# Kernel tuning notes

Hardware: AMD Instinct MI355X
Metric: run time of the kernel (lower is better)

Reference implementation:

```python
import jax, jax.numpy as jnp
import numpy as np

B, T, VG, S = 64, 256, 1232, 32
LW, VW = 64, 8000
N_TAGS = 8
BLANK = 0
IGNORE_INDEX = 0
TAG_FACTOR = 0.1
GLOSS_W = 1.0
WORD_W = 1.0
NEG = -1e30


def setup_inputs() -> dict:
    key = jax.random.key(0)
    k1, k2, k3, k4, k5, k6 = jax.random.split(key, 6)
    glosses = jax.random.randint(k1, (B, S), 1, VG)            # CTC targets (avoid blank=0)
    words = jax.random.randint(k2, (B, LW), 0, VW)             # translation targets
    glosses_scores = jax.random.normal(k3, (B, T, VG), jnp.float32)
    words_output = jax.nn.log_softmax(jax.random.normal(k4, (B, LW, VW), jnp.float32), axis=-1)
    frames_len = jnp.full((B,), T, jnp.int32)
    glosses_len = jax.random.randint(k5, (B,), 1, S + 1).astype(jnp.int32)
    tag_ids = jax.random.randint(k6, (VG,), 0, N_TAGS).astype(jnp.int32)
    return {"glosses": glosses, "words": words, "glosses_scores": glosses_scores,
            "words_output": words_output, "frames_len": frames_len,
            "glosses_len": glosses_len, "tag_ids": tag_ids}


def booster_scores(scores, tag_ids):
    # per-tag mean over vocab dim, gathered back per vocab entry
    onehot = jax.nn.one_hot(tag_ids, N_TAGS, dtype=scores.dtype)   # [V, n_tags]
    counts = onehot.sum(axis=0)                                    # [n_tags]
    tag_mean = jnp.einsum('btv,vn->btn', scores, onehot) / counts  # [B,T,n_tags]
    return scores + TAG_FACTOR * tag_mean[..., tag_ids]            # [B,T,V]


def ctc_loss_sum(log_probs, targets, input_lens, target_lens):
    # log_probs [B,T,V], targets [B,S]
    Bb, Tt, _ = log_probs.shape
    Ss = targets.shape[1]
    L = 2 * Ss + 1
    ext = jnp.full((Bb, L), BLANK, dtype=targets.dtype).at[:, 1::2].set(targets)  # blank-interleaved
    lp_ext = jnp.take_along_axis(log_probs, jnp.broadcast_to(ext[:, None, :], (Bb, Tt, L)), axis=2)  # [B,T,L]
    prev2 = jnp.pad(ext, ((0, 0), (2, 0)), constant_values=BLANK)[:, :L]
    can_skip = (ext != BLANK) & (ext != prev2)                    # [B,L]

    alpha0 = jnp.full((Bb, L), NEG, log_probs.dtype)
    alpha0 = alpha0.at[:, 0].set(lp_ext[:, 0, 0]).at[:, 1].set(lp_ext[:, 0, 1])

    lp_t = jnp.swapaxes(lp_ext, 0, 1)  # [T,B,L]

    def step(alpha, xs):
        lp, t = xs
        a1 = jnp.concatenate([jnp.full((Bb, 1), NEG, alpha.dtype), alpha[:, :-1]], axis=1)
        a2 = jnp.concatenate([jnp.full((Bb, 2), NEG, alpha.dtype), alpha[:, :-2]], axis=1)
        a2 = jnp.where(can_skip, a2, NEG)
        m = jnp.maximum(alpha, jnp.maximum(a1, a2))
        new = m + jnp.log(jnp.exp(alpha - m) + jnp.exp(a1 - m) + jnp.exp(a2 - m)) + lp
        valid = (t < input_lens)[:, None]
        return jnp.where(valid, new, alpha), None

    alpha, _ = jax.lax.scan(step, alpha0, (lp_t[1:], jnp.arange(1, Tt)))

    idx1 = 2 * target_lens.astype(jnp.int32)
    idx0 = jnp.maximum(idx1 - 1, 0)
    aN = jnp.take_along_axis(alpha, jnp.stack([idx0, idx1], axis=1), axis=1)  # [B,2]
    loss = -jax.nn.logsumexp(aN, axis=1)
    loss = jnp.where(loss > 1e29, 0.0, loss)  # zero_infinity
    return loss.sum()


def nll_loss_sum(log_probs, targets):
    # input = words_output.permute(0,2,1)[:,:,:-1], target = words[:,1:]
    lp = log_probs[:, :-1, :]          # [B, LW-1, VW]
    tgt = targets[:, 1:]               # [B, LW-1]
    g = jnp.take_along_axis(lp, tgt[..., None], axis=2)[..., 0]
    mask = tgt != IGNORE_INDEX
    return -jnp.where(mask, g, 0.0).sum()


def reference(glosses, words, glosses_scores, words_output, frames_len, glosses_len, tag_ids):
    boosted = booster_scores(glosses_scores, tag_ids)          # training=True path
    glosses_probs = jax.nn.log_softmax(boosted, axis=-1)
    recognition_loss = ctc_loss_sum(glosses_probs, glosses, frames_len, glosses_len)
    translation_loss = nll_loss_sum(words_output, words)
    total = GLOSS_W * recognition_loss + WORD_W * translation_loss
    return (total, recognition_loss, translation_loss)
```

## Files before the change

kernel.cpp:

```cpp
#include <hip/hip_runtime.h>

#define B_    64
#define T_    256
#define VG_   1232
#define S_    32
#define LW_   64
#define VW_   8000
#define NTAGS 8
#define NEG_  (-1e30f)
#define LP_STRIDE 34
#define LOG2E 1.44269504088896340736f
#define LN2   0.69314718055994530942f

__device__ __forceinline__ float exp2g(float x) {
    float r; asm("v_exp_f32 %0, %1" : "=v"(r) : "v"(x)); return r;
}
__device__ __forceinline__ float log2g(float x) {
    float r; asm("v_log_f32 %0, %1" : "=v"(r) : "v"(x)); return r;
}
__device__ __forceinline__ void st_agent(float* p, float v) {
    __hip_atomic_store(p, v, __ATOMIC_RELAXED, __HIP_MEMORY_SCOPE_AGENT);
}
__device__ __forceinline__ float ld_agent(const float* p) {
    return __hip_atomic_load(p, __ATOMIC_RELAXED, __HIP_MEMORY_SCOPE_AGENT);
}
__device__ __forceinline__ float dpp_shr1(float x, float fill) {
    int r = __builtin_amdgcn_update_dpp(
        __builtin_bit_cast(int, fill), __builtin_bit_cast(int, x),
        0x138, 0xF, 0xF, false);
    return __builtin_bit_cast(float, r);
}
template <int CTRL>
__device__ __forceinline__ float dpp_add(float x) {
    int s = __builtin_amdgcn_update_dpp(
        0, __builtin_bit_cast(int, x), CTRL, 0xF, 0xF, true);
    return x + __builtin_bit_cast(float, s);
}
__device__ __forceinline__ float wave_sum_to0(float x) {
    x = dpp_add<0x101>(x);
    x = dpp_add<0x102>(x);
    x = dpp_add<0x104>(x);
    x = dpp_add<0x108>(x);
    x += __shfl_xor(x, 16, 64);
    x += __shfl_xor(x, 32, 64);
    return x;
}

__global__ void k0_counts(const int* __restrict__ tag_ids,
                          float* __restrict__ invcnt2, int* __restrict__ counter) {
    __shared__ int c[NTAGS];
    if (threadIdx.x == 0) *counter = 0;
    if (threadIdx.x < NTAGS) c[threadIdx.x] = 0;
    __syncthreads();
    for (int v = threadIdx.x; v < VG_; v += 256)
        atomicAdd(&c[tag_ids[v]], 1);
    __syncthreads();
    if (threadIdx.x < NTAGS)
        invcnt2[threadIdx.x] = (0.1f * LOG2E) / (float)c[threadIdx.x];
}

__global__ __launch_bounds__(256) void kA_booster(
    const float* __restrict__ scores, const int* __restrict__ tag_ids,
    const int* __restrict__ glosses, const float* __restrict__ invcnt2,
    float* __restrict__ lp_ws)
{
    __shared__ float tm2L[4][NTAGS];
    const int tid  = threadIdx.x;
    const int lane = tid & 63;
    const int wv   = tid >> 6;
    const int row  = blockIdx.x * 4 + wv;
    const int b    = row >> 8;
    const float* srow = scores + (size_t)row * VG_;

    const int gidx = (lane >= 1 && lane < 33) ? glosses[b * S_ + lane - 1] : 0;

    float4 sv[5];
    int4   tv[5];
#pragma unroll
    for (int i = 0; i < 5; ++i) {
        const int idx = i * 64 + lane;
        const bool act = (i < 4) || (lane < 52);
        sv[i] = act ? ((const float4*)srow)[idx]  : make_float4(0.f, 0.f, 0.f, 0.f);
        tv[i] = act ? ((const int4*)tag_ids)[idx] : make_int4(0, 0, 0, 0);
    }
    const float gval = srow[gidx];
    const int   gtag = tag_ids[gidx];

    float sums[NTAGS];
#pragma unroll
    for (int n = 0; n < NTAGS; ++n) sums[n] = 0.f;
#pragma unroll
    for (int i = 0; i < 5; ++i) {
        const float xs[4] = {sv[i].x, sv[i].y, sv[i].z, sv[i].w};
        const int   ts[4] = {tv[i].x, tv[i].y, tv[i].z, tv[i].w};
#pragma unroll
        for (int j = 0; j < 4; ++j) {
#pragma unroll
            for (int n = 0; n < NTAGS; ++n)
                sums[n] += (ts[j] == n) ? xs[j] : 0.f;
        }
    }
#pragma unroll
    for (int n = 0; n < NTAGS; ++n) sums[n] = wave_sum_to0(sums[n]);

    if (lane == 0) {
#pragma unroll
        for (int n = 0; n < NTAGS; ++n)
            tm2L[wv][n] = sums[n] * invcnt2[n];
    }
    __builtin_amdgcn_sched_barrier(0);

    float se = 0.f;
#pragma unroll
    for (int i = 0; i < 5; ++i) {
        const float xs[4] = {sv[i].x, sv[i].y, sv[i].z, sv[i].w};
        const int   ts[4] = {tv[i].x, tv[i].y, tv[i].z, tv[i].w};
        const bool act = (i < 4) || (lane < 52);
#pragma unroll
        for (int j = 0; j < 4; ++j) {
            const float e = exp2g(fmaf(xs[j], LOG2E, tm2L[wv][ts[j]]));
            se += act ? e : 0.f;
        }
    }
    se = wave_sum_to0(se);
    const float se0 = __builtin_bit_cast(
        float, __builtin_amdgcn_readfirstlane(__builtin_bit_cast(int, se)));
    const float lse2 = log2g(se0);

    if (lane < 33) {
        const float v = fmaf(gval, LOG2E, tm2L[wv][gtag]) - lse2;
        lp_ws[(size_t)row * LP_STRIDE + lane] = v;
    }
}

template <bool FULL>
__device__ __forceinline__ void scan_body(
    const float* __restrict__ tile, int lane, int off, bool ok2, int Tlen,
    float& alpha, float& a64)
{
    auto STEP = [&](int t, float lp, float lpB) {
        const float a1 = dpp_shr1(alpha, NEG_);
        float a2 = dpp_shr1(a1, NEG_);
        a2 = ok2 ? a2 : NEG_;
        const float m3 = fmaxf(alpha, fmaxf(a1, a2));
        const float e0 = exp2g(alpha - m3);
        const float e1 = exp2g(a1 - m3);
        const float e2 = exp2g(a2 - m3);
        const float nw = (m3 + lp) + log2g((e0 + e1) + e2);
        const float m2 = fmaxf(a64, alpha);
        const float n64 = (m2 + lpB) + log2g(exp2g(a64 - m2) + exp2g(alpha - m2));
        if (FULL || t < Tlen) { alpha = nw; a64 = n64; }
    };

    float cur[4], curB[4];
#pragma unroll
    for (int j = 0; j < 4; ++j) {
        cur[j]  = tile[(1 + j) * LP_STRIDE + off];
        curB[j] = tile[(1 + j) * LP_STRIDE];
    }
    int tbase = 1;
    for (int g = 0; g < 63; ++g) {
        float nxt[4], nxtB[4];
        const int tb2 = tbase + 4;
#pragma unroll
        for (int j = 0; j < 4; ++j) {
            nxt[j]  = tile[(tb2 + j) * LP_STRIDE + off];
            nxtB[j] = tile[(tb2 + j) * LP_STRIDE];
        }
#pragma unroll
        for (int j = 0; j < 4; ++j) STEP(tbase + j, cur[j], curB[j]);
#pragma unroll
        for (int j = 0; j < 4; ++j) { cur[j] = nxt[j]; curB[j] = nxtB[j]; }
        tbase += 4;
    }
#pragma unroll
    for (int j = 0; j < 3; ++j) STEP(253 + j, cur[j], curB[j]);
}

__global__ __launch_bounds__(256) void kB_ctc_nll_final(
    const float* __restrict__ lp_ws, const int* __restrict__ glosses,
    const int* __restrict__ frames_len, const int* __restrict__ glosses_len,
    const int* __restrict__ words, const float* __restrict__ words_out,
    float* __restrict__ loss_ws, float* __restrict__ nll_ws,
    int* __restrict__ counter, float* __restrict__ out)
{
    __shared__ __align__(16) float tile[(T_ + 1) * LP_STRIDE];
    const int tid = threadIdx.x;
    const int b   = blockIdx.x;

    float nacc = 0.f;
    if (tid < LW_ - 1) {
        const int tgt = words[b * LW_ + tid + 1];
        if (tgt != 0)
            nacc = -words_out[((size_t)b * LW_ + tid) * VW_ + tgt];
    }

    {
        const float4* src4 = (const float4*)(lp_ws + (size_t)b * T_ * LP_STRIDE);
        float4* dst4 = (float4*)tile;
        float4 r[9];
#pragma unroll
        for (int i = 0; i < 9; ++i) {
            const int idx = i * 256 + tid;
            if (idx < 2176) r[i] = src4[idx];
        }
#pragma unroll
        for (int i = 0; i < 9; ++i) {
            const int idx = i * 256 + tid;
            if (idx < 2176) dst4[idx] = r[i];
        }
    }
    __syncthreads();
    if (tid >= 64) return;
    const int lane = tid;

    const bool odd  = (lane & 1) != 0;
    const int  sIdx = (lane - 1) >> 1;
    bool ok2 = false;
    if (odd && sIdx >= 1) {
        const int g  = glosses[b * S_ + sIdx];
        const int gp = glosses[b * S_ + sIdx - 1];
        ok2 = (g != gp) && (g != 0);
    }
    const int off = odd ? (1 + sIdx) : 0;

    float alpha = NEG_;
    float a64   = NEG_;
    {
        const float lp00 = tile[off];
        if (lane <= 1) alpha = lp00;
    }
    const int Tlen = frames_len[b];

    if (Tlen == T_) scan_body<true >(tile, lane, off, ok2, Tlen, alpha, a64);
    else            scan_body<false>(tile, lane, off, ok2, Tlen, alpha, a64);

    const float a64v = __shfl(a64, 63, 64);
    const int i1 = 2 * glosses_len[b];
    const int i0 = i1 - 1;
    const float A0 = __shfl(alpha, i0, 64);
    const float A1 = (i1 >= 64) ? a64v : __shfl(alpha, i1, 64);
    const float mm = fmaxf(A0, A1);
    float loss = -(mm + log2g(exp2g(A0 - mm) + exp2g(A1 - mm))) * LN2;
    if (loss > 1e29f) loss = 0.f;

    nacc = wave_sum_to0(nacc);
    if (lane == 0) {
        st_agent(&loss_ws[b], loss);
        st_agent(&nll_ws[b], nacc);
    }

    asm volatile("s_waitcnt vmcnt(0)" ::: "memory");
    int old = 0;
    if (lane == 0) old = atomicAdd(counter, 1);
    old = __shfl(old, 0, 64);
    if (old == B_ - 1) {
        float v = ld_agent(&loss_ws[lane]);
        float u = ld_agent(&nll_ws[lane]);
#pragma unroll
        for (int o = 32; o >= 1; o >>= 1) {
            v += __shfl_xor(v, o, 64);
            u += __shfl_xor(u, o, 64);
        }
        if (lane == 0) {
            out[0] = v + u;
            out[1] = v;
            out[2] = u;
        }
    }
}

extern "C" void kernel_launch(void* const* d_in, const int* in_sizes, int n_in,
                              void* d_out, int out_size, void* d_ws, size_t ws_size,
                              hipStream_t stream) {
    const int*   glosses     = (const int*)d_in[0];
    const int*   words       = (const int*)d_in[1];
    const float* scores      = (const float*)d_in[2];
    const float* words_out   = (const float*)d_in[3];
    const int*   frames_len  = (const int*)d_in[4];
    const int*   glosses_len = (const int*)d_in[5];
    const int*   tag_ids     = (const int*)d_in[6];
    float* out = (float*)d_out;

    float* w       = (float*)d_ws;
    int*   counter = (int*)d_ws;
    float* invcnt2 = w + 8;
    float* loss_ws = w + 16;
    float* nll_ws  = w + 96;
    float* lp_ws   = w + 192;

    k0_counts<<<1, 256, 0, stream>>>(tag_ids, invcnt2, counter);
    kA_booster<<<(B_ * T_) / 4, 256, 0, stream>>>(scores, tag_ids, glosses,
                                                  invcnt2, lp_ws);
    kB_ctc_nll_final<<<B_, 256, 0, stream>>>(lp_ws, glosses, frames_len,
                                             glosses_len, words, words_out,
                                             loss_ws, nll_ws, counter, out);
}
```

Measured before the change: 52.19 us.

## Replace log-space CTC recursion with mantissa/exponent scaled probability-space scan

Rewrites the CTC alpha recursion to keep each state as a float mantissa plus an integer exponent in linear probability space, instead of log-space values. Each step now uses ldexp, add, multiply and frexp in place of several exp2 and log2 transcendental calls, which shortens the serial dependency chain of the latency-bound single-wave scan. Emission probabilities are exponentiated once as they are loaded. It adds integer DPP shifts and extra register state, and it changes numerical behaviour, so a NaN guard was added to the final loss.

```diff
diff --git a/kernel.cpp b/kernel.cpp
--- a/kernel.cpp
+++ b/kernel.cpp
@@ -8,6 +8,7 @@
 #define VW_   8000
 #define NTAGS 8
 #define NEG_  (-1e30f)
+#define RNEG  (-(1 << 28))
 #define LP_STRIDE 34
 #define LOG2E 1.44269504088896340736f
 #define LN2   0.69314718055994530942f
@@ -17,6 +18,15 @@
 }
 __device__ __forceinline__ float log2g(float x) {
     float r; asm("v_log_f32 %0, %1" : "=v"(r) : "v"(x)); return r;
+}
+__device__ __forceinline__ float ldexpg(float x, int e) {
+    float r; asm("v_ldexp_f32 %0, %1, %2" : "=v"(r) : "v"(x), "v"(e)); return r;
+}
+__device__ __forceinline__ float frexp_mantg(float x) {
+    float r; asm("v_frexp_mant_f32 %0, %1" : "=v"(r) : "v"(x)); return r;
+}
+__device__ __forceinline__ int frexp_expg(float x) {
+    int r; asm("v_frexp_exp_i32_f32 %0, %1" : "=v"(r) : "v"(x)); return r;
 }
 __device__ __forceinline__ void st_agent(float* p, float v) {
     __hip_atomic_store(p, v, __ATOMIC_RELAXED, __HIP_MEMORY_SCOPE_AGENT);
@@ -29,6 +39,9 @@
         __builtin_bit_cast(int, fill), __builtin_bit_cast(int, x),
         0x138, 0xF, 0xF, false);
     return __builtin_bit_cast(float, r);
+}
+__device__ __forceinline__ int dpp_shr1_i(int x, int fill) {
+    return __builtin_amdgcn_update_dpp(fill, x, 0x138, 0xF, 0xF, false);
 }
 template <int CTRL>
 __device__ __forceinline__ float dpp_add(float x) {
@@ -134,29 +147,34 @@
 }
 
 template <bool FULL>
-__device__ __forceinline__ void scan_body(
+__device__ __forceinline__ void scan_body_pls(
     const float* __restrict__ tile, int lane, int off, bool ok2, int Tlen,
-    float& alpha, float& a64)
+    float& mant, int& Rl, float& m64, int& R64)
 {
-    auto STEP = [&](int t, float lp, float lpB) {
-        const float a1 = dpp_shr1(alpha, NEG_);
-        float a2 = dpp_shr1(a1, NEG_);
-        a2 = ok2 ? a2 : NEG_;
-        const float m3 = fmaxf(alpha, fmaxf(a1, a2));
-        const float e0 = exp2g(alpha - m3);
-        const float e1 = exp2g(a1 - m3);
-        const float e2 = exp2g(a2 - m3);
-        const float nw = (m3 + lp) + log2g((e0 + e1) + e2);
-        const float m2 = fmaxf(a64, alpha);
-        const float n64 = (m2 + lpB) + log2g(exp2g(a64 - m2) + exp2g(alpha - m2));
-        if (FULL || t < Tlen) { alpha = nw; a64 = n64; }
+    auto STEP = [&](int t, float p, float pB) {
+        const float m1 = dpp_shr1(mant, 0.f);
+        const int   r1 = dpp_shr1_i(Rl, RNEG);
+        float m2 = dpp_shr1(m1, 0.f);
+        int   r2 = dpp_shr1_i(r1, RNEG);
+        m2 = ok2 ? m2 : 0.f;
+        r2 = ok2 ? r2 : RNEG;
+        const int rmax = max(Rl, max(r1, r2));
+        const float s  = ((ldexpg(mant, Rl - rmax) + ldexpg(m1, r1 - rmax))
+                          + ldexpg(m2, r2 - rmax)) * p;
+        const int   rb = max(R64, Rl);
+        const float sb = (ldexpg(m64, R64 - rb) + ldexpg(mant, Rl - rb)) * pB;
+        const float nm  = frexp_mantg(s);
+        const int   nr  = rmax + frexp_expg(s);
+        const float nmb = frexp_mantg(sb);
+        const int   nrb = rb + frexp_expg(sb);
+        if (FULL || t < Tlen) { mant = nm; Rl = nr; m64 = nmb; R64 = nrb; }
     };
 
     float cur[4], curB[4];
 #pragma unroll
     for (int j = 0; j < 4; ++j) {
-        cur[j]  = tile[(1 + j) * LP_STRIDE + off];
-        curB[j] = tile[(1 + j) * LP_STRIDE];
+        cur[j]  = exp2g(tile[(1 + j) * LP_STRIDE + off]);
+        curB[j] = exp2g(tile[(1 + j) * LP_STRIDE]);
     }
     int tbase = 1;
     for (int g = 0; g < 63; ++g) {
@@ -170,7 +188,9 @@
 #pragma unroll
         for (int j = 0; j < 4; ++j) STEP(tbase + j, cur[j], curB[j]);
 #pragma unroll
-        for (int j = 0; j < 4; ++j) { cur[j] = nxt[j]; curB[j] = nxtB[j]; }
+        for (int j = 0; j < 4; ++j) {
+            cur[j] = exp2g(nxt[j]); curB[j] = exp2g(nxtB[j]);
+        }
         tbase += 4;
     }
 #pragma unroll
@@ -224,25 +244,31 @@
     }
     const int off = odd ? (1 + sIdx) : 0;
 
-    float alpha = NEG_;
-    float a64   = NEG_;
+    float mant; int Rl;
     {
-        const float lp00 = tile[off];
-        if (lane <= 1) alpha = lp00;
-    }
+        const float a0 = (lane <= 1) ? exp2g(tile[off]) : 0.f;
+        mant = frexp_mantg(a0);
+        Rl   = (lane <= 1) ? frexp_expg(a0) : RNEG;
+    }
+    float m64 = 0.f; int R64 = RNEG;
     const int Tlen = frames_len[b];
 
-    if (Tlen == T_) scan_body<true >(tile, lane, off, ok2, Tlen, alpha, a64);
-    else            scan_body<false>(tile, lane, off, ok2, Tlen, alpha, a64);
-
-    const float a64v = __shfl(a64, 63, 64);
+    if (Tlen == T_) scan_body_pls<true >(tile, lane, off, ok2, Tlen, mant, Rl, m64, R64);
+    else            scan_body_pls<false>(tile, lane, off, ok2, Tlen, mant, Rl, m64, R64);
+
+    const float m64v = __shfl(m64, 63, 64);
+    const int   R64v = __shfl(R64, 63, 64);
     const int i1 = 2 * glosses_len[b];
     const int i0 = i1 - 1;
-    const float A0 = __shfl(alpha, i0, 64);
-    const float A1 = (i1 >= 64) ? a64v : __shfl(alpha, i1, 64);
-    const float mm = fmaxf(A0, A1);
-    float loss = -(mm + log2g(exp2g(A0 - mm) + exp2g(A1 - mm))) * LN2;
+    const float mA0 = __shfl(mant, i0, 64);
+    const int   rA0 = __shfl(Rl,   i0, 64);
+    const float mA1 = (i1 >= 64) ? m64v : __shfl(mant, i1, 64);
+    const int   rA1 = (i1 >= 64) ? R64v : __shfl(Rl,   i1, 64);
+    const int   rf  = max(rA0, rA1);
+    const float ssum = ldexpg(mA0, rA0 - rf) + ldexpg(mA1, rA1 - rf);
+    float loss = -(log2g(ssum) + (float)rf) * LN2;
     if (loss > 1e29f) loss = 0.f;
+    if (!(loss == loss)) loss = 0.f;
 
     nacc = wave_sum_to0(nacc);
     if (lane == 0) {
```

New measurement: 54.14 us. 1.04x slower.
